# Optimization experiments

Measured on AMD Instinct MI355X. Metric: run time of the kernel, lower is better.

Reference implementation:

```python
import jax, jax.numpy as jnp
import numpy as np
import math

V, E, H, L, HID, T, B = 32000, 1024, 16, 4, 4096, 1024, 4
HS = E // H  # head size = 64


def _ln(x, g, b, eps=1e-5):
    m = jnp.mean(x, axis=-1, keepdims=True)
    v = jnp.var(x, axis=-1, keepdims=True)
    return (x - m) * jax.lax.rsqrt(v + eps) * g + b


def _pos_encoding(t, e):
    pos = jnp.arange(t, dtype=jnp.float32)[:, None]
    div = jnp.exp(jnp.arange(0, e, 2, dtype=jnp.float32) * (-math.log(10000.0) / e))
    pe = jnp.zeros((t, e), dtype=jnp.float32)
    pe = pe.at[:, 0::2].set(jnp.sin(pos * div))
    pe = pe.at[:, 1::2].set(jnp.cos(pos * div))
    return pe


def setup_inputs() -> dict:
    key = jax.random.key(0)
    ks = jax.random.split(key, 16)
    std = 0.02
    inp = {
        'idx': jax.random.randint(ks[0], (B, T), 0, V),
        'targets': jax.random.randint(ks[1], (B, T), 0, V),
        'tok_emb': jax.random.normal(ks[2], (V, E), jnp.float32) * std,
        'ln1_g': jnp.ones((L, E), jnp.float32),
        'ln1_b': jnp.zeros((L, E), jnp.float32),
        'wq': jax.random.normal(ks[3], (L, H, E, HS), jnp.float32) * std,
        'wk': jax.random.normal(ks[4], (L, H, E, HS), jnp.float32) * std,
        'wv': jax.random.normal(ks[5], (L, H, E, HS), jnp.float32) * std,
        'wo': jax.random.normal(ks[6], (L, H * HS, E), jnp.float32) * std,
        'bo': jnp.zeros((L, E), jnp.float32),
        'ln2_g': jnp.ones((L, E), jnp.float32),
        'ln2_b': jnp.zeros((L, E), jnp.float32),
        'w1': jax.random.normal(ks[7], (L, E, HID), jnp.float32) * std,
        'b1': jnp.zeros((L, HID), jnp.float32),
        'w2': jax.random.normal(ks[8], (L, HID, E), jnp.float32) * std,
        'b2': jnp.zeros((L, E), jnp.float32),
        'lnf_g': jnp.ones((E,), jnp.float32),
        'lnf_b': jnp.zeros((E,), jnp.float32),
        'lm_w': jax.random.normal(ks[9], (E, V), jnp.float32) * std,
        'lm_b': jnp.zeros((V,), jnp.float32),
    }
    return inp


def _forward(idx, targets, tok_emb, ln1_g, ln1_b, wq, wk, wv, wo, bo,
             ln2_g, ln2_b, w1, b1, w2, b2, lnf_g, lnf_b, lm_w, lm_b):
    b, t = idx.shape
    x = tok_emb[idx] * math.sqrt(E)              # [B,T,E], scaled embedding
    x = x + _pos_encoding(t, E)                  # sinusoidal pos enc
    causal = jnp.tril(jnp.ones((t, t), dtype=bool))
    scale = HS ** -0.5
    for l in range(L):
        h = _ln(x, ln1_g[l], ln1_b[l])
        q = jnp.einsum('bte,hek->bhtk', h, wq[l])
        k = jnp.einsum('bte,hek->bhtk', h, wk[l])
        v = jnp.einsum('bte,hek->bhtk', h, wv[l])
        scores = jnp.einsum('bhtk,bhsk->bhts', q, k) * scale
        scores = jnp.where(causal, scores, -jnp.inf)
        w = jax.nn.softmax(scores, axis=-1)
        o = jnp.einsum('bhts,bhsk->bhtk', w, v)
        o = o.transpose(0, 2, 1, 3).reshape(b, t, H * HS)  # concat heads
        x = x + o @ wo[l] + bo[l]
        h2 = _ln(x, ln2_g[l], ln2_b[l])
        x = x + jax.nn.relu(h2 @ w1[l] + b1[l]) @ w2[l] + b2[l]
    x = _ln(x, lnf_g, lnf_b)
    logits = x @ lm_w + lm_b                     # [B,T,V]
    logp = jax.nn.log_softmax(logits, axis=-1)
    loss = -jnp.mean(jnp.take_along_axis(logp, targets[..., None], axis=-1))
    return logits, loss


def reference(idx, targets, tok_emb, ln1_g, ln1_b, wq, wk, wv, wo, bo,
              ln2_g, ln2_b, w1, b1, w2, b2, lnf_g, lnf_b, lm_w, lm_b):
    return _forward(idx, targets, tok_emb, ln1_g, ln1_b, wq, wk, wv, wo, bo,
                    ln2_g, ln2_b, w1, b1, w2, b2, lnf_g, lnf_b, lm_w, lm_b)
```

## Files before the change

### kernel.cpp

```cpp
#include <hip/hip_runtime.h>
#include <hip/hip_bf16.h>
#include <math.h>

#define BB 4
#define TT 1024
#define BT 4096
#define EE 1024
#define HH 16
#define HSZ 64
#define LL 4
#define HID 4096
#define VV 32000
#define LOG2E 1.44269504f

typedef __attribute__((ext_vector_type(8))) __bf16 bf16x8;
typedef __attribute__((ext_vector_type(4))) float f32x4;

#define MFMA16(a, b, c) __builtin_amdgcn_mfma_f32_16x16x32_bf16((a), (b), (c), 0, 0, 0)

__device__ __forceinline__ int swz32(int row, int chunk) {
    return row * 32 + ((chunk ^ ((row >> 1) & 3)) << 3);
}

__device__ __forceinline__ void gload16(const __bf16* g, __bf16* l) {
    __builtin_amdgcn_global_load_lds(
        (const __attribute__((address_space(1))) unsigned int*)g,
        (__attribute__((address_space(3))) unsigned int*)l, 16, 0, 0);
}

__global__ __launch_bounds__(256) void transpose_conv(
    const float* __restrict__ in, __bf16* __restrict__ out,
    int R, int C, long ibs, int bdiv, long os1, long os2)
{
    __shared__ __bf16 tile[64][65];
    const int t = threadIdx.x;
    const int c0 = blockIdx.x * 64, r0 = blockIdx.y * 64;
    const int batch = blockIdx.z;
    const float* ib = in + (size_t)batch * ibs;
    __bf16* ob = out + (size_t)(batch / bdiv) * os1 + (size_t)(batch % bdiv) * os2;
#pragma unroll
    for (int p = 0; p < 4; ++p) {
        const int r = (t >> 4) + p * 16;
        const int c = (t & 15) * 4;
        float4 v = *(const float4*)(ib + (size_t)(r0 + r) * C + c0 + c);
        tile[c + 0][r] = (__bf16)v.x;
        tile[c + 1][r] = (__bf16)v.y;
        tile[c + 2][r] = (__bf16)v.z;
        tile[c + 3][r] = (__bf16)v.w;
    }
    __syncthreads();
#pragma unroll
    for (int p = 0; p < 2; ++p) {
        const int g = t + p * 256;
        const int co = g >> 3, ch = g & 7;
        bf16x8 vv;
#pragma unroll
        for (int j = 0; j < 8; ++j) vv[j] = tile[co][ch * 8 + j];
        *(bf16x8*)(ob + (size_t)(c0 + co) * R + r0 + ch * 8) = vv;
    }
}

__global__ __launch_bounds__(256) void embed_kernel(
    const int* __restrict__ idx, const float* __restrict__ emb, float* __restrict__ x)
{
    const int row = blockIdx.x, tid = threadIdx.x;
    const float pos = (float)(row & (TT - 1));
    const int tok = idx[row];
    const int cb = tid * 4;
    float4 ev = *(const float4*)(emb + (size_t)tok * EE + cb);
    const float kk = -9.2103403720f / (float)EE;
    float pe[4];
#pragma unroll
    for (int j = 0; j < 4; ++j) {
        const int c = cb + j;
        const float div = expf(kk * (float)(c & ~1));
        const float ang = pos * div;
        pe[j] = (c & 1) ? cosf(ang) : sinf(ang);
    }
    float4 r;
    r.x = ev.x * 32.0f + pe[0];
    r.y = ev.y * 32.0f + pe[1];
    r.z = ev.z * 32.0f + pe[2];
    r.w = ev.w * 32.0f + pe[3];
    *(float4*)(x + (size_t)row * EE + cb) = r;
}

__global__ __launch_bounds__(256) void ln_kernel(
    const float* __restrict__ x, const float* __restrict__ g,
    const float* __restrict__ be, __bf16* __restrict__ out)
{
    __shared__ float red[2][4];
    const int row = blockIdx.x, tid = threadIdx.x;
    float4 v = *(const float4*)(x + (size_t)row * EE + tid * 4);
    float s = v.x + v.y + v.z + v.w;
    float ss = v.x * v.x + v.y * v.y + v.z * v.z + v.w * v.w;
#pragma unroll
    for (int m = 1; m < 64; m <<= 1) { s += __shfl_xor(s, m); ss += __shfl_xor(ss, m); }
    if ((tid & 63) == 0) { red[0][tid >> 6] = s; red[1][tid >> 6] = ss; }
    __syncthreads();
    s  = red[0][0] + red[0][1] + red[0][2] + red[0][3];
    ss = red[1][0] + red[1][1] + red[1][2] + red[1][3];
    const float mean = s * (1.0f / EE);
    const float var  = ss * (1.0f / EE) - mean * mean;
    const float rs   = rsqrtf(var + 1e-5f);
    float4 gv = *(const float4*)(g + tid * 4);
    float4 bv = *(const float4*)(be + tid * 4);
    __bf16* o = out + (size_t)row * EE + tid * 4;
    o[0] = (__bf16)((v.x - mean) * rs * gv.x + bv.x);
    o[1] = (__bf16)((v.y - mean) * rs * gv.y + bv.y);
    o[2] = (__bf16)((v.z - mean) * rs * gv.z + bv.z);
    o[3] = (__bf16)((v.w - mean) * rs * gv.w + bv.w);
}

template <int MODE, int BN>
__global__ __launch_bounds__(256, 2) void gemm_bt(
    const __bf16* __restrict__ A, const __bf16* __restrict__ Bt,
    const float* __restrict__ bias, float* __restrict__ C,
    __bf16* __restrict__ Cb, int M, int N, int K)
{
    constexpr int JW  = BN / 32;
    constexpr int BSW = BN / 64;
    __shared__ __bf16 As[128 * 32];
    __shared__ __bf16 Bs[BN * 32];

    const int tid = threadIdx.x;
    const int lane = tid & 63, wid = tid >> 6;
    const int wr = wid >> 1, wc = wid & 1;
    const int m0 = blockIdx.y * 128, n0 = blockIdx.x * BN;

    size_t sA[2];  int loA[2];
#pragma unroll
    for (int c = 0; c < 2; ++c) {
        const int seg = wid * 2 + c;
        const int rl = seg * 16 + (lane >> 2);
        const int cl = (lane & 3) ^ ((rl >> 1) & 3);
        loA[c] = seg * 512;
        sA[c] = (size_t)(m0 + rl) * K + cl * 8;
    }
    size_t sB[BSW]; int loB[BSW];
#pragma unroll
    for (int c = 0; c < BSW; ++c) {
        const int seg = wid * BSW + c;
        const int rl = seg * 16 + (lane >> 2);
        const int cl = (lane & 3) ^ ((rl >> 1) & 3);
        loB[c] = seg * 512;
        sB[c] = (size_t)(n0 + rl) * K + cl * 8;
    }

    const int l15 = lane & 15, kch = lane >> 4;
    const int abase = swz32(wr * 64 + l15, kch);
    const int bbase = swz32(wc * (BN / 2) + l15, kch);

    f32x4 acc[4][JW] = {};

    const int nk = K >> 5;
    for (int kt = 0; kt < nk; ++kt) {
        const size_t ko = (size_t)kt * 32;
#pragma unroll
        for (int c = 0; c < 2; ++c)   gload16(A + sA[c] + ko, As + loA[c]);
#pragma unroll
        for (int c = 0; c < BSW; ++c) gload16(Bt + sB[c] + ko, Bs + loB[c]);
        __syncthreads();
        bf16x8 af[4], bfr[JW];
#pragma unroll
        for (int i = 0; i < 4; ++i)  af[i]  = *(const bf16x8*)(As + abase + i * 512);
#pragma unroll
        for (int j = 0; j < JW; ++j) bfr[j] = *(const bf16x8*)(Bs + bbase + j * 512);
#pragma unroll
        for (int i = 0; i < 4; ++i)
#pragma unroll
            for (int j = 0; j < JW; ++j)
                acc[i][j] = MFMA16(af[i], bfr[j], acc[i][j]);
        __syncthreads();
    }

    const int crow = m0 + wr * 64 + ((lane >> 4) << 2);
    const int ccol = n0 + wc * (BN / 2) + l15;
#pragma unroll
    for (int i = 0; i < 4; ++i)
#pragma unroll
        for (int j = 0; j < JW; ++j) {
            const int cc = ccol + j * 16;
#pragma unroll
            for (int r = 0; r < 4; ++r) {
                const size_t oidx = (size_t)(crow + i * 16 + r) * N + cc;
                float v = acc[i][j][r];
                if (MODE == 0) {
                    Cb[oidx] = (__bf16)v;
                } else if (MODE == 1) {
                    v += bias[cc];
                    Cb[oidx] = (__bf16)(v > 0.0f ? v : 0.0f);
                } else if (MODE == 2) {
                    C[oidx] += v + bias[cc];
                } else {
                    C[oidx] = v + bias[cc];
                }
            }
        }
}

template <int MODE, int GSWZ>
__global__ __launch_bounds__(512, 2) void gemm_bt2(
    const __bf16* __restrict__ A, const __bf16* __restrict__ Bt,
    const float* __restrict__ bias, float* __restrict__ C,
    __bf16* __restrict__ Cb, float2* __restrict__ part,
    int M, int N, int K)
{
    __shared__ __bf16 As[256 * 32];
    __shared__ __bf16 Bs[128 * 32];
    __shared__ float2 red[(MODE == 4) ? 256 : 1][2];

    const int tid = threadIdx.x;
    const int lane = tid & 63, wid = tid >> 6;
    const int wm = wid >> 1, wn = wid & 1;
    int bm, bn;
    if (GSWZ) {
        const int b = blockIdx.x;
        const int j = b >> 3;
        bm = (b & 7) * 2 + (j & 1);
        bn = j >> 1;
    } else {
        bm = blockIdx.y; bn = blockIdx.x;
    }
    const int m0 = bm * 256, n0 = bn * 128;
    const int l15 = lane & 15, lg = lane >> 4;

    size_t sA[2];  int loA[2];
#pragma unroll
    for (int c = 0; c < 2; ++c) {
        const int seg = wid * 2 + c;
        const int rl = seg * 16 + (lane >> 2);
        const int cl = (lane & 3) ^ ((rl >> 1) & 3);
        loA[c] = seg * 512;
        sA[c] = (size_t)(m0 + rl) * K + cl * 8;
    }
    size_t sB;  int loB;
    {
        const int rl = wid * 16 + (lane >> 2);
        const int cl = (lane & 3) ^ ((rl >> 1) & 3);
        loB = wid * 512;
        sB = (size_t)(n0 + rl) * K + cl * 8;
    }

    const int abase = swz32(wm * 64 + l15, lg);
    const int bbase = swz32(wn * 64 + l15, lg);

    f32x4 acc[4][4] = {};

    const int nk = K >> 5;
    for (int kt = 0; kt < nk; ++kt) {
        const size_t ko = (size_t)kt * 32;
        gload16(A + sA[0] + ko, As + loA[0]);
        gload16(A + sA[1] + ko, As + loA[1]);
        gload16(Bt + sB + ko, Bs + loB);
        __syncthreads();
        bf16x8 af[4], bfr[4];
#pragma unroll
        for (int i = 0; i < 4; ++i) af[i]  = *(const bf16x8*)(As + abase + i * 512);
#pragma unroll
        for (int j = 0; j < 4; ++j) bfr[j] = *(const bf16x8*)(Bs + bbase + j * 512);
#pragma unroll
        for (int i = 0; i < 4; ++i)
#pragma unroll
            for (int j = 0; j < 4; ++j)
                acc[i][j] = MFMA16(af[i], bfr[j], acc[i][j]);
        __syncthreads();
    }

    const int crow = m0 + wm * 64 + lg * 4;
    const int ccol = n0 + wn * 64 + l15;
#pragma unroll
    for (int i = 0; i < 4; ++i)
#pragma unroll
        for (int j = 0; j < 4; ++j) {
            const int cc = ccol + j * 16;
#pragma unroll
            for (int r = 0; r < 4; ++r) {
                const size_t oidx = (size_t)(crow + i * 16 + r) * N + cc;
                float v = acc[i][j][r];
                if (MODE == 0) {
                    Cb[oidx] = (__bf16)v;
                } else if (MODE == 1) {
                    v += bias[cc];
                    Cb[oidx] = (__bf16)(v > 0.0f ? v : 0.0f);
                } else {
                    C[oidx] = v + bias[cc];
                }
            }
        }

    if constexpr (MODE == 4) {
#pragma unroll
        for (int i = 0; i < 4; ++i)
#pragma unroll
            for (int r = 0; r < 4; ++r) {
                float tv[4];
                float mx = -1e30f;
#pragma unroll
                for (int j = 0; j < 4; ++j) {
                    tv[j] = acc[i][j][r] + bias[ccol + j * 16];
                    mx = fmaxf(mx, tv[j]);
                }
                mx = fmaxf(mx, __shfl_xor(mx, 1));
                mx = fmaxf(mx, __shfl_xor(mx, 2));
                mx = fmaxf(mx, __shfl_xor(mx, 4));
                mx = fmaxf(mx, __shfl_xor(mx, 8));
                float sm = 0.0f;
#pragma unroll
                for (int j = 0; j < 4; ++j) sm += exp2f((tv[j] - mx) * LOG2E);
                sm += __shfl_xor(sm, 1);
                sm += __shfl_xor(sm, 2);
                sm += __shfl_xor(sm, 4);
                sm += __shfl_xor(sm, 8);
                if (l15 == 0)
                    red[wm * 64 + i * 16 + lg * 4 + r][wn] = make_float2(mx, sm);
            }
        __syncthreads();
        if (tid < 256) {
            const float2 a = red[tid][0], b2 = red[tid][1];
            const float M2 = fmaxf(a.x, b2.x);
            const float S = a.y * exp2f((a.x - M2) * LOG2E)
                          + b2.y * exp2f((b2.x - M2) * LOG2E);
            part[(size_t)(m0 + tid) * (N >> 7) + bn] = make_float2(M2, S);
        }
    }
}

__global__ __launch_bounds__(64) void attn_kernel(
    const __bf16* __restrict__ qkv, __bf16* __restrict__ out)
{
    __shared__ __bf16 Pl[16 * 32];
    __shared__ __bf16 Vt[64 * 32];
    const int lane = threadIdx.x;
    const int bh = blockIdx.x, b = bh >> 4, hh = bh & 15;
    const int qbase = blockIdx.y * 16;
    const int RS = 3 * EE;
    const __bf16* qp = qkv + (size_t)(b * TT) * RS + hh * HSZ;
    const __bf16* kp = qp + EE;
    const __bf16* vp = qp + 2 * EE;
    const int l15 = lane & 15, lg = lane >> 4;

    bf16x8 aq[2];
#pragma unroll
    for (int e = 0; e < 2; ++e)
        aq[e] = *(const bf16x8*)(qp + (size_t)(qbase + l15) * RS + e * 32 + lg * 8);

    f32x4 ao[4] = {};
    float mrun[4], lrun[4];
#pragma unroll
    for (int r = 0; r < 4; ++r) { mrun[r] = -1e30f; lrun[r] = 0.0f; }

    const int ntile = qbase / 32 + 1;
    for (int st = 0; st < ntile; ++st) {
        const int sbase = st * 32;
        f32x4 as[2] = {};
        __builtin_amdgcn_s_setprio(1);
#pragma unroll
        for (int n = 0; n < 2; ++n)
#pragma unroll
            for (int e = 0; e < 2; ++e) {
                bf16x8 bk = *(const bf16x8*)(kp + (size_t)(sbase + n * 16 + l15) * RS + e * 32 + lg * 8);
                as[n] = MFMA16(aq[e], bk, as[n]);
            }
        __builtin_amdgcn_s_setprio(0);
        {
            const int sl = lane >> 1;
            const int e0 = (lane & 1) * 32;
            const __bf16* vr = vp + (size_t)(sbase + sl) * RS + e0;
#pragma unroll
            for (int c = 0; c < 4; ++c) {
                bf16x8 vvv = *(const bf16x8*)(vr + c * 8);
#pragma unroll
                for (int j = 0; j < 8; ++j)
                    Vt[swz32(e0 + c * 8 + j, sl >> 3) + (sl & 7)] = vvv[j];
            }
        }
#pragma unroll
        for (int r = 0; r < 4; ++r) {
            const int qi = qbase + lg * 4 + r;
            float sc0 = as[0][r] * 0.125f;
            float sc1 = as[1][r] * 0.125f;
            if (sbase + l15 > qi)      sc0 = -1e30f;
            if (sbase + 16 + l15 > qi) sc1 = -1e30f;
            float rm = fmaxf(sc0, sc1);
            rm = fmaxf(rm, __shfl_xor(rm, 1));
            rm = fmaxf(rm, __shfl_xor(rm, 2));
            rm = fmaxf(rm, __shfl_xor(rm, 4));
            rm = fmaxf(rm, __shfl_xor(rm, 8));
            const float mnew = fmaxf(mrun[r], rm);
            const float alpha = exp2f((mrun[r] - mnew) * LOG2E);
            const float p0 = exp2f((sc0 - mnew) * LOG2E);
            const float p1 = exp2f((sc1 - mnew) * LOG2E);
            float rs = p0 + p1;
            rs += __shfl_xor(rs, 1);
            rs += __shfl_xor(rs, 2);
            rs += __shfl_xor(rs, 4);
            rs += __shfl_xor(rs, 8);
            lrun[r] = lrun[r] * alpha + rs;
            mrun[r] = mnew;
#pragma unroll
            for (int n = 0; n < 4; ++n) ao[n][r] *= alpha;
            const int prow = lg * 4 + r;
            Pl[swz32(prow, l15 >> 3) + (l15 & 7)] = (__bf16)p0;
            Pl[swz32(prow, (16 + l15) >> 3) + (l15 & 7)] = (__bf16)p1;
        }
        asm volatile("s_waitcnt lgkmcnt(0)" ::: "memory");
        bf16x8 pa = *(const bf16x8*)(&Pl[swz32(l15, lg)]);
        __builtin_amdgcn_s_setprio(1);
#pragma unroll
        for (int n = 0; n < 4; ++n) {
            bf16x8 bv = *(const bf16x8*)(&Vt[swz32(n * 16 + l15, lg)]);
            ao[n] = MFMA16(pa, bv, ao[n]);
        }
        __builtin_amdgcn_s_setprio(0);
        asm volatile("s_waitcnt lgkmcnt(0)" ::: "memory");
    }
#pragma unroll
    for (int r = 0; r < 4; ++r) {
        const float inv = 1.0f / lrun[r];
        const int row = qbase + lg * 4 + r;
#pragma unroll
        for (int n = 0; n < 4; ++n)
            out[(size_t)(b * TT + row) * EE + hh * HSZ + n * 16 + l15] =
                (__bf16)(ao[n][r] * inv);
    }
}

__global__ __launch_bounds__(256) void loss_reduce(
    const float2* __restrict__ part, const float* __restrict__ logits,
    const int* __restrict__ tgt, float* __restrict__ lossv, int NP)
{
    __shared__ float rm[4], rs2[4];
    const int row = blockIdx.x, tid = threadIdx.x;
    float m = -1e30f, s = 0.0f;
    if (tid < NP) {
        const float2 p = part[(size_t)row * NP + tid];
        m = p.x; s = p.y;
    }
#pragma unroll
    for (int k = 1; k < 64; k <<= 1) {
        const float mo = __shfl_xor(m, k), so = __shfl_xor(s, k);
        const float mn = fmaxf(m, mo);
        s = s * exp2f((m - mn) * LOG2E) + so * exp2f((mo - mn) * LOG2E);
        m = mn;
    }
    if ((tid & 63) == 0) { rm[tid >> 6] = m; rs2[tid >> 6] = s; }
    __syncthreads();
    if (tid == 0) {
        float M = rm[0];
#pragma unroll
        for (int w = 1; w < 4; ++w) M = fmaxf(M, rm[w]);
        float S = 0.0f;
#pragma unroll
        for (int w = 0; w < 4; ++w) S += rs2[w] * exp2f((rm[w] - M) * LOG2E);
        lossv[row] = M + logf(S) - logits[(size_t)row * VV + tgt[row]];
    }
}

__global__ __launch_bounds__(256) void loss_final(const float* __restrict__ lossv, float* __restrict__ out)
{
    __shared__ float red[4];
    const int tid = threadIdx.x;
    float s = 0.0f;
    for (int i = tid; i < BT; i += 256) s += lossv[i];
#pragma unroll
    for (int k = 1; k < 64; k <<= 1) s += __shfl_xor(s, k);
    if ((tid & 63) == 0) red[tid >> 6] = s;
    __syncthreads();
    if (tid == 0) out[0] = (red[0] + red[1] + red[2] + red[3]) * (1.0f / BT);
}

extern "C" void kernel_launch(void* const* d_in, const int* in_sizes, int n_in,
                              void* d_out, int out_size, void* d_ws, size_t ws_size,
                              hipStream_t stream)
{
    const int*   idx   = (const int*)d_in[0];
    const int*   tgt   = (const int*)d_in[1];
    const float* temb  = (const float*)d_in[2];
    const float* ln1g  = (const float*)d_in[3];
    const float* ln1b  = (const float*)d_in[4];
    const float* wq    = (const float*)d_in[5];
    const float* wk    = (const float*)d_in[6];
    const float* wv    = (const float*)d_in[7];
    const float* wo    = (const float*)d_in[8];
    const float* bo    = (const float*)d_in[9];
    const float* ln2g  = (const float*)d_in[10];
    const float* ln2b  = (const float*)d_in[11];
    const float* w1    = (const float*)d_in[12];
    const float* b1    = (const float*)d_in[13];
    const float* w2    = (const float*)d_in[14];
    const float* b2    = (const float*)d_in[15];
    const float* lnfg  = (const float*)d_in[16];
    const float* lnfb  = (const float*)d_in[17];
    const float* lm_w  = (const float*)d_in[18];
    const float* lm_b  = (const float*)d_in[19];

    float* logits  = (float*)d_out;
    float* lossout = logits + (size_t)BT * VV;

    char* ws = (char*)d_ws;
    size_t off = 0;
    auto carve = [&](size_t bytes) {
        void* p = ws + off;
        off += (bytes + 255) & ~(size_t)255;
        return p;
    };
    __bf16* WQKVT = (__bf16*)carve((size_t)LL * 3072 * 1024 * 2);
    __bf16* WOT   = (__bf16*)carve((size_t)LL * 1024 * 1024 * 2);
    __bf16* W1T   = (__bf16*)carve((size_t)LL * 4096 * 1024 * 2);
    __bf16* W2T   = (__bf16*)carve((size_t)LL * 1024 * 4096 * 2);
    __bf16* LMT   = (__bf16*)carve((size_t)VV * 1024 * 2);
    float*  x     = (float*)carve((size_t)BT * EE * 4);
    __bf16* h     = (__bf16*)carve((size_t)BT * EE * 2);
    __bf16* qkv   = (__bf16*)carve((size_t)BT * 3072 * 2);
    __bf16* mid   = (__bf16*)carve((size_t)BT * HID * 2);
    float*  lossv = (float*)carve((size_t)BT * 4);
    float2* part  = (float2*)mid;

    const dim3 blk(256);

    transpose_conv<<<dim3(1, 16, 64), blk, 0, stream>>>(wq, WQKVT,           1024, 64,   65536, 16, 3145728, 65536);
    transpose_conv<<<dim3(1, 16, 64), blk, 0, stream>>>(wk, WQKVT + 1048576, 1024, 64,   65536, 16, 3145728, 65536);
    transpose_conv<<<dim3(1, 16, 64), blk, 0, stream>>>(wv, WQKVT + 2097152, 1024, 64,   65536, 16, 3145728, 65536);
    transpose_conv<<<dim3(16, 16, 4), blk, 0, stream>>>(wo, WOT,   1024, 1024, 1048576, 4, 0, 1048576);
    transpose_conv<<<dim3(64, 16, 4), blk, 0, stream>>>(w1, W1T,   1024, 4096, 4194304, 4, 0, 4194304);
    transpose_conv<<<dim3(16, 64, 4), blk, 0, stream>>>(w2, W2T,   4096, 1024, 4194304, 4, 0, 4194304);
    transpose_conv<<<dim3(500, 16, 1), blk, 0, stream>>>(lm_w, LMT, 1024, 32000, 0, 1, 0, 0);

    embed_kernel<<<BT, blk, 0, stream>>>(idx, temb, x);

    for (int l = 0; l < LL; ++l) {
        ln_kernel<<<BT, blk, 0, stream>>>(x, ln1g + l * EE, ln1b + l * EE, h);
        gemm_bt2<0, 0><<<dim3(24, 16), dim3(512), 0, stream>>>(h, WQKVT + (size_t)l * 3145728,
                                                               nullptr, nullptr, qkv, nullptr, BT, 3072, 1024);
        attn_kernel<<<dim3(64, 64), dim3(64), 0, stream>>>(qkv, h);
        gemm_bt<2, 64><<<dim3(16, 32), blk, 0, stream>>>(h, WOT + (size_t)l * 1048576,
                                                         bo + l * EE, x, nullptr, BT, 1024, 1024);
        ln_kernel<<<BT, blk, 0, stream>>>(x, ln2g + l * EE, ln2b + l * EE, h);
        gemm_bt2<1, 0><<<dim3(32, 16), dim3(512), 0, stream>>>(h, W1T + (size_t)l * 4194304,
                                                               b1 + l * HID, nullptr, mid, nullptr, BT, 4096, 1024);
        gemm_bt<2, 64><<<dim3(16, 32), blk, 0, stream>>>(mid, W2T + (size_t)l * 4194304,
                                                         b2 + l * EE, x, nullptr, BT, 1024, 4096);
    }
    ln_kernel<<<BT, blk, 0, stream>>>(x, lnfg, lnfb, h);
    gemm_bt2<4, 1><<<dim3(4000), dim3(512), 0, stream>>>(h, LMT, lm_b, logits, nullptr, part, BT, VV, 1024);
    loss_reduce<<<BT, blk, 0, stream>>>(part, logits, tgt, lossv, VV >> 7);
    loss_final<<<1, blk, 0, stream>>>(lossv, lossout);
}
```

Baseline: 1.674 ms.

## Deepen GEMM K-step to 64 and switch QKV projection to 128x128 tile kernel

Both bf16 MFMA GEMM kernels now stage two 32-wide K slices into shared memory per iteration, halving the number of barrier pairs per K sweep and giving more MFMAs between syncs. The QKV projection also moves from the 256x128 gemm_bt2 kernel to gemm_bt with BN=128, doubling the grid to 768 blocks for better CU occupancy. The cost is doubled LDS per block, which may reduce blocks resident per CU, and there is still no real software pipelining of loads against compute.

```diff
diff --git a/kernel.cpp b/kernel.cpp
--- a/kernel.cpp
+++ b/kernel.cpp
@@ -120,8 +120,8 @@
 {
     constexpr int JW  = BN / 32;
     constexpr int BSW = BN / 64;
-    __shared__ __bf16 As[128 * 32];
-    __shared__ __bf16 Bs[BN * 32];
+    __shared__ __bf16 As[2][128 * 32];
+    __shared__ __bf16 Bs[2][BN * 32];
 
     const int tid = threadIdx.x;
     const int lane = tid & 63, wid = tid >> 6;
@@ -153,24 +153,32 @@
 
     f32x4 acc[4][JW] = {};
 
-    const int nk = K >> 5;
+    const int nk = K >> 6;
     for (int kt = 0; kt < nk; ++kt) {
-        const size_t ko = (size_t)kt * 32;
-#pragma unroll
-        for (int c = 0; c < 2; ++c)   gload16(A + sA[c] + ko, As + loA[c]);
-#pragma unroll
-        for (int c = 0; c < BSW; ++c) gload16(Bt + sB[c] + ko, Bs + loB[c]);
+        const size_t ko = (size_t)kt * 64;
+#pragma unroll
+        for (int kh = 0; kh < 2; ++kh) {
+#pragma unroll
+            for (int c = 0; c < 2; ++c)
+                gload16(A + sA[c] + ko + kh * 32, &As[kh][loA[c]]);
+#pragma unroll
+            for (int c = 0; c < BSW; ++c)
+                gload16(Bt + sB[c] + ko + kh * 32, &Bs[kh][loB[c]]);
+        }
         __syncthreads();
-        bf16x8 af[4], bfr[JW];
-#pragma unroll
-        for (int i = 0; i < 4; ++i)  af[i]  = *(const bf16x8*)(As + abase + i * 512);
-#pragma unroll
-        for (int j = 0; j < JW; ++j) bfr[j] = *(const bf16x8*)(Bs + bbase + j * 512);
-#pragma unroll
-        for (int i = 0; i < 4; ++i)
-#pragma unroll
-            for (int j = 0; j < JW; ++j)
-                acc[i][j] = MFMA16(af[i], bfr[j], acc[i][j]);
+#pragma unroll
+        for (int kh = 0; kh < 2; ++kh) {
+            bf16x8 af[4], bfr[JW];
+#pragma unroll
+            for (int i = 0; i < 4; ++i)  af[i]  = *(const bf16x8*)(&As[kh][abase + i * 512]);
+#pragma unroll
+            for (int j = 0; j < JW; ++j) bfr[j] = *(const bf16x8*)(&Bs[kh][bbase + j * 512]);
+#pragma unroll
+            for (int i = 0; i < 4; ++i)
+#pragma unroll
+                for (int j = 0; j < JW; ++j)
+                    acc[i][j] = MFMA16(af[i], bfr[j], acc[i][j]);
+        }
         __syncthreads();
     }
 
@@ -206,8 +214,8 @@
     __bf16* __restrict__ Cb, float2* __restrict__ part,
     int M, int N, int K)
 {
-    __shared__ __bf16 As[256 * 32];
-    __shared__ __bf16 Bs[128 * 32];
+    __shared__ __bf16 As[2][256 * 32];
+    __shared__ __bf16 Bs[2][128 * 32];
     __shared__ float2 red[(MODE == 4) ? 256 : 1][2];
 
     const int tid = threadIdx.x;
@@ -247,23 +255,29 @@
 
     f32x4 acc[4][4] = {};
 
-    const int nk = K >> 5;
+    const int nk = K >> 6;
     for (int kt = 0; kt < nk; ++kt) {
-        const size_t ko = (size_t)kt * 32;
-        gload16(A + sA[0] + ko, As + loA[0]);
-        gload16(A + sA[1] + ko, As + loA[1]);
-        gload16(Bt + sB + ko, Bs + loB);
+        const size_t ko = (size_t)kt * 64;
+#pragma unroll
+        for (int kh = 0; kh < 2; ++kh) {
+            gload16(A + sA[0] + ko + kh * 32, &As[kh][loA[0]]);
+            gload16(A + sA[1] + ko + kh * 32, &As[kh][loA[1]]);
+            gload16(Bt + sB + ko + kh * 32, &Bs[kh][loB]);
+        }
         __syncthreads();
-        bf16x8 af[4], bfr[4];
-#pragma unroll
-        for (int i = 0; i < 4; ++i) af[i]  = *(const bf16x8*)(As + abase + i * 512);
-#pragma unroll
-        for (int j = 0; j < 4; ++j) bfr[j] = *(const bf16x8*)(Bs + bbase + j * 512);
-#pragma unroll
-        for (int i = 0; i < 4; ++i)
-#pragma unroll
-            for (int j = 0; j < 4; ++j)
-                acc[i][j] = MFMA16(af[i], bfr[j], acc[i][j]);
+#pragma unroll
+        for (int kh = 0; kh < 2; ++kh) {
+            bf16x8 af[4], bfr[4];
+#pragma unroll
+            for (int i = 0; i < 4; ++i) af[i]  = *(const bf16x8*)(&As[kh][abase + i * 512]);
+#pragma unroll
+            for (int j = 0; j < 4; ++j) bfr[j] = *(const bf16x8*)(&Bs[kh][bbase + j * 512]);
+#pragma unroll
+            for (int i = 0; i < 4; ++i)
+#pragma unroll
+                for (int j = 0; j < 4; ++j)
+                    acc[i][j] = MFMA16(af[i], bfr[j], acc[i][j]);
+        }
         __syncthreads();
     }
 
@@ -531,8 +545,8 @@
 
     for (int l = 0; l < LL; ++l) {
         ln_kernel<<<BT, blk, 0, stream>>>(x, ln1g + l * EE, ln1b + l * EE, h);
-        gemm_bt2<0, 0><<<dim3(24, 16), dim3(512), 0, stream>>>(h, WQKVT + (size_t)l * 3145728,
-                                                               nullptr, nullptr, qkv, nullptr, BT, 3072, 1024);
+        gemm_bt<0, 128><<<dim3(24, 32), blk, 0, stream>>>(h, WQKVT + (size_t)l * 3145728,
+                                                          nullptr, nullptr, qkv, BT, 3072, 1024);
         attn_kernel<<<dim3(64, 64), dim3(64), 0, stream>>>(qkv, h);
         gemm_bt<2, 64><<<dim3(16, 32), blk, 0, stream>>>(h, WOT + (size_t)l * 1048576,
                                                          bo + l * EE, x, nullptr, BT, 1024, 1024);
```

New measurement: 1.635 ms. 2.3% less time.
